# Kernel tuning notes

Measured on AMD Instinct MI355X. Metric: run time of the kernel, lower is better.

## Reference

```python
import jax, jax.numpy as jnp
import numpy as np

# TensorProductConvLayer (DiffDock-style): gather -> edge-MLP-weighted fully
# connected tensor product (lmax=1 irreps) -> scatter-mean.
# in/out irreps: ns x0e + nv x1o + nv x1e + ns x0o ; sh irreps: 1x0e + 1x1o
NS, NV = 16, 4
N_NODES, N_EDGES = 8000, 160000
EDGE_FEAT = 3 * NS                      # 48
IRREPS_DIM = 2 * NS + 6 * NV            # 56
# per-path weight block sizes (fully-connected 'uvw' paths, mul2 = 1):
# [A:0e*0e->0e, B:1o*1o->0e, A:0e*1o->1o, B:1o*0e->1o, C:1e*1o->1o,
#  B:1o*1o->1e, C:1e*0e->1e, D:0o*1o->1e, C:1e*1o->0o, D:0o*0e->0o]
PATH_SIZES = [NS*NS, NV*NS, NS*NV, NV*NV, NV*NV, NV*NV, NV*NV, NS*NV, NV*NS, NS*NS]
W_NUMEL = sum(PATH_SIZES)               # 832
# component-normalized CG factors: 1x1->0 uses delta/sqrt(3); 1x1->1 uses eps/sqrt(2)
INV_SQRT3 = float(1.0 / np.sqrt(3.0))
INV_SQRT2 = float(1.0 / np.sqrt(2.0))
# element path normalization: 1/sqrt(total fan-in mul per output irrep)
A_SCAL = float(1.0 / np.sqrt(NS + NV))      # 0e / 0o outputs
A_VEC = float(1.0 / np.sqrt(NS + 2 * NV))   # 1o / 1e outputs


def setup_inputs() -> dict:
    key = jax.random.key(0)
    ks = jax.random.split(key, 6)
    node_attr = jax.random.normal(ks[0], (N_NODES, IRREPS_DIM), jnp.float32)
    edge_index = jax.random.randint(ks[1], (2, N_EDGES), 0, N_NODES)
    edge_attr = jax.random.normal(ks[2], (N_EDGES, EDGE_FEAT), jnp.float32)
    edge_sh = jax.random.normal(ks[3], (N_EDGES, 4), jnp.float32)
    s = float(1.0 / np.sqrt(EDGE_FEAT))
    fc_w1 = jax.random.normal(ks[4], (EDGE_FEAT, EDGE_FEAT), jnp.float32) * s
    fc_b1 = jnp.zeros((EDGE_FEAT,), jnp.float32)
    fc_w2 = jax.random.normal(ks[5], (EDGE_FEAT, W_NUMEL), jnp.float32) * s
    fc_b2 = jnp.zeros((W_NUMEL,), jnp.float32)
    return dict(node_attr=node_attr, edge_attr=edge_attr, edge_sh=edge_sh,
                fc_w1=fc_w1, fc_b1=fc_b1, fc_w2=fc_w2, fc_b2=fc_b2,
                edge_index=edge_index)


def _split_weights(w):
    outs, off = [], 0
    for sz in PATH_SIZES:
        outs.append(w[:, off:off + sz])
        off += sz
    return outs


def _tp_conv(node_attr, edge_attr, edge_sh, fc_w1, fc_b1, fc_w2, fc_b2, src, dst):
    # edge MLP -> per-edge tensor-product weights [E, 832]
    h = jax.nn.relu(edge_attr @ fc_w1 + fc_b1)
    w = h @ fc_w2 + fc_b2
    wA0, wB0, wA1, wB1, wC1, wB1e, wC1e, wD1e, wC0o, wD0o = _split_weights(w)

    x = node_attr[dst]                         # gather [E, 56]
    x0e = x[:, :NS]
    x1o = x[:, NS:NS + 3 * NV].reshape(-1, NV, 3)
    x1e = x[:, NS + 3 * NV:NS + 6 * NV].reshape(-1, NV, 3)
    x0o = x[:, NS + 6 * NV:]
    s0 = edge_sh[:, 0]
    s1 = edge_sh[:, 1:4]

    # ---- 0e output [E, ns]
    o0e = jnp.einsum('eu,euv->ev', x0e, wA0.reshape(-1, NS, NS)) * s0[:, None]
    dot_b = jnp.einsum('eui,ei->eu', x1o, s1) * INV_SQRT3   # 1o x 1o -> 0e
    o0e = (o0e + jnp.einsum('eu,euv->ev', dot_b, wB0.reshape(-1, NV, NS))) * A_SCAL

    # ---- 1o output [E, nv, 3]
    o1o = jnp.einsum('eu,euv->ev', x0e, wA1.reshape(-1, NS, NV))[:, :, None] * s1[:, None, :]
    o1o = o1o + jnp.einsum('eui,euv->evi', x1o, wB1.reshape(-1, NV, NV)) * s0[:, None, None]
    cr_e = jnp.cross(x1e, s1[:, None, :]) * INV_SQRT2       # 1e x 1o -> 1o
    o1o = (o1o + jnp.einsum('eui,euv->evi', cr_e, wC1.reshape(-1, NV, NV))) * A_VEC

    # ---- 1e output [E, nv, 3]
    cr_o = jnp.cross(x1o, s1[:, None, :]) * INV_SQRT2       # 1o x 1o -> 1e
    o1e = jnp.einsum('eui,euv->evi', cr_o, wB1e.reshape(-1, NV, NV))
    o1e = o1e + jnp.einsum('eui,euv->evi', x1e, wC1e.reshape(-1, NV, NV)) * s0[:, None, None]
    o1e = (o1e + jnp.einsum('eu,euv->ev', x0o, wD1e.reshape(-1, NS, NV))[:, :, None] * s1[:, None, :]) * A_VEC

    # ---- 0o output [E, ns]
    dot_c = jnp.einsum('eui,ei->eu', x1e, s1) * INV_SQRT3   # 1e x 1o -> 0o
    o0o = jnp.einsum('eu,euv->ev', dot_c, wC0o.reshape(-1, NV, NS))
    o0o = (o0o + jnp.einsum('eu,euv->ev', x0o, wD0o.reshape(-1, NS, NS)) * s0[:, None]) * A_SCAL

    tp = jnp.concatenate([o0e, o1o.reshape(-1, 3 * NV), o1e.reshape(-1, 3 * NV), o0o], axis=-1)

    # scatter-mean over source nodes
    summed = jax.ops.segment_sum(tp, src, num_segments=N_NODES)
    counts = jax.ops.segment_sum(jnp.ones((tp.shape[0],), tp.dtype), src, num_segments=N_NODES)
    return summed / jnp.maximum(counts, 1.0)[:, None]


def reference(node_attr, edge_attr, edge_sh, fc_w1, fc_b1, fc_w2, fc_b2, edge_index):
    src, dst = edge_index[0], edge_index[1]
    return _tp_conv(node_attr, edge_attr, edge_sh, fc_w1, fc_b1, fc_w2, fc_b2, src, dst)
```

## Files before the change

kernel.cpp:

```cpp
#include <hip/hip_runtime.h>
#include <hip/hip_fp16.h>

#define IRR    56
#define EF     48
#define WN     832
#define NEDGE  160000
#define NNODE  8000
#define NT     512
#define TE2    64
#define NTASK  (NEDGE / TE2)
#define GRID   NTASK

#define INV_SQRT3 0.5773502691896258f
#define INV_SQRT2 0.7071067811865476f
#define A_SCAL    0.22360679774997896f
#define A_VEC     0.20412414523193154f

typedef __bf16 bf16x8 __attribute__((ext_vector_type(8)));
typedef float  f32x4  __attribute__((ext_vector_type(4)));
typedef unsigned short u16x8 __attribute__((ext_vector_type(8)));
typedef unsigned short u16x4 __attribute__((ext_vector_type(4)));

__device__ __forceinline__ unsigned short f2bf(float f) {
    unsigned int u = __builtin_bit_cast(unsigned int, f);
    u += 0x7FFFu + ((u >> 16) & 1u);
    return (unsigned short)(u >> 16);
}

__global__ void k_setup(const float* __restrict__ w1, const float* __restrict__ b1,
                        const float* __restrict__ w2, const float* __restrict__ b2,
                        unsigned short* __restrict__ W1T, unsigned short* __restrict__ W2L,
                        const int* __restrict__ edge_index, int* __restrict__ hist)
{
    int o = blockIdx.x * 256 + threadIdx.x;
    if (o < 64 * 832) {
        int k = o / 832;
        int n = o - k * 832;
        float v = (k < EF) ? w2[k * WN + n] : ((k == EF) ? b2[n] : 0.f);
        int i = n >> 4, mm = n & 15;
        int f = k >> 5, q = (k >> 3) & 3, j = k & 7;
        int o2 = (((i * 2 + f) * 64) + (q * 16 + mm)) * 8 + j;
        W2L[o2] = f2bf(v);
    }
    if (o < EF * EF) { int k = o / EF, n = o - k * EF; W1T[n * 64 + k] = f2bf(w1[o]); }
    if (o < EF * 16) { int n = o >> 4, kk = EF + (o & 15); W1T[n * 64 + kk] = (kk == EF) ? f2bf(b1[n]) : (unsigned short)0; }
    if (o < NEDGE) atomicAdd(&hist[edge_index[o]], 1);
}

__global__ __launch_bounds__(NT, 4) void tp_fused(
    const float* __restrict__ node_attr,
    const float* __restrict__ edge_attr,
    const float* __restrict__ edge_sh,
    const int*   __restrict__ edge_index,
    const int*   __restrict__ hist,
    const unsigned short* __restrict__ W1T,
    const unsigned short* __restrict__ W2L,
    float* __restrict__ out)
{
    __shared__ __align__(16) unsigned char UGH[TE2 * 56 * 4];
    __shared__ __align__(16) float sF0[TE2 * 61];
    __shared__ __align__(16) float sF1[TE2 * 61];
    __shared__ __align__(16) float sO[TE2 * IRR];
    __shared__ int   sSrc[TE2], sDst[TE2];
    __shared__ float sInv[TE2];

    float*          sG = (float*)UGH;
    unsigned short* sH = (unsigned short*)UGH;

    const int tid   = threadIdx.x;
    const int lane  = tid & 63;
    const int wv    = tid >> 6;
    const int half  = wv >> 2;
    const int wl    = wv & 3;
    const int m     = lane & 15;
    const int quad  = lane >> 4;
    const int em    = wl * 16 + m;
    const int e0    = blockIdx.x * TE2;

    if (tid < TE2)          sSrc[tid]       = edge_index[e0 + tid];
    else if (tid < 2 * TE2) sDst[tid - TE2] = edge_index[NEDGE + e0 + tid - TE2];
    __syncthreads();

    {
        const float* nrow = node_attr + (size_t)sDst[em] * IRR;
        float* g = sG + em * 56;
        if (half == 0) {
            *(float4*)(g + quad * 4)        = *(const float4*)(nrow + quad * 4);
            *(float4*)(g + (quad + 4) * 4)  = *(const float4*)(nrow + (quad + 4) * 4);
        } else {
            *(float4*)(g + (quad + 8) * 4)  = *(const float4*)(nrow + (quad + 8) * 4);
            if (quad < 2) { int c = 12 + quad; *(float4*)(g + c * 4) = *(const float4*)(nrow + c * 4); }
        }
    }
    if (tid >= 256 && tid < 256 + TE2) {
        int e = tid - 256;
        sInv[e] = 1.0f / fmaxf((float)hist[sSrc[e]], 1.0f);
    }

    float4 sh4 = *(const float4*)&edge_sh[(size_t)(e0 + em) * 4];
    const float s0 = sh4.x, sx = sh4.y, sy = sh4.z, sz = sh4.w;

    __syncthreads();

    {
        const float* x = sG + em * 56;
        const float c0S = s0 * A_SCAL;
        const float c0V = s0 * A_VEC;
        const float cD3 = INV_SQRT3 * A_SCAL;
        const float cC2 = INV_SQRT2 * A_VEC;
        if (half == 0) {
            float* F = sF0 + em * 61;
            #pragma unroll
            for (int t = 0; t < 4; t++) {
                int u = quad * 4 + t;
                float x0e = x[u];
                F[u]      = x0e * c0S;
                F[20 + u] = x0e * A_VEC;
            }
            {
                int u = quad;
                float a0 = x[16 + u*3], a1 = x[16 + u*3 + 1], a2 = x[16 + u*3 + 2];
                float b0 = x[28 + u*3], b1 = x[28 + u*3 + 1], b2 = x[28 + u*3 + 2];
                F[16 + u] = (a0*sx + a1*sy + a2*sz) * cD3;
                F[36 + u*3 + 0] = a0 * c0V;
                F[36 + u*3 + 1] = a1 * c0V;
                F[36 + u*3 + 2] = a2 * c0V;
                F[48 + u*3 + 0] = (b1*sz - b2*sy) * cC2;
                F[48 + u*3 + 1] = (b2*sx - b0*sz) * cC2;
                F[48 + u*3 + 2] = (b0*sy - b1*sx) * cC2;
            }
        } else {
            float* F = sF1 + em * 61;
            {
                int u = quad;
                float a0 = x[16 + u*3], a1 = x[16 + u*3 + 1], a2 = x[16 + u*3 + 2];
                float b0 = x[28 + u*3], b1 = x[28 + u*3 + 1], b2 = x[28 + u*3 + 2];
                F[u*3 + 0]      = (a1*sz - a2*sy) * cC2;
                F[u*3 + 1]      = (a2*sx - a0*sz) * cC2;
                F[u*3 + 2]      = (a0*sy - a1*sx) * cC2;
                F[12 + u*3 + 0] = b0 * c0V;
                F[12 + u*3 + 1] = b1 * c0V;
                F[12 + u*3 + 2] = b2 * c0V;
                F[40 + u]       = (b0*sx + b1*sy + b2*sz) * cD3;
            }
            #pragma unroll
            for (int t = 0; t < 4; t++) {
                int u = quad * 4 + t;
                float x0o = x[40 + u];
                F[24 + u] = x0o * A_VEC;
                F[44 + u] = x0o * c0S;
            }
        }
    }

    bf16x8 hb0, hb1;
    if (half == 0) {
        const float* arow = edge_attr + (size_t)(e0 + em) * EF;
        float av0[8], av1[8];
        {
            float4 p0 = *(const float4*)(arow + quad * 8);
            float4 p1 = *(const float4*)(arow + quad * 8 + 4);
            av0[0]=p0.x; av0[1]=p0.y; av0[2]=p0.z; av0[3]=p0.w;
            av0[4]=p1.x; av0[5]=p1.y; av0[6]=p1.z; av0[7]=p1.w;
        }
        if (quad < 2) {
            float4 p0 = *(const float4*)(arow + 32 + quad * 8);
            float4 p1 = *(const float4*)(arow + 32 + quad * 8 + 4);
            av1[0]=p0.x; av1[1]=p0.y; av1[2]=p0.z; av1[3]=p0.w;
            av1[4]=p1.x; av1[5]=p1.y; av1[6]=p1.z; av1[7]=p1.w;
        } else {
            #pragma unroll
            for (int j = 0; j < 8; j++) av1[j] = 0.f;
            if (quad == 2) av1[0] = 1.f;
        }
        u16x8 ub0, ub1;
        #pragma unroll
        for (int j = 0; j < 8; j++) { ub0[j] = f2bf(av0[j]); ub1[j] = f2bf(av1[j]); }
        hb0 = __builtin_bit_cast(bf16x8, ub0);
        hb1 = __builtin_bit_cast(bf16x8, ub1);
    }

    __syncthreads();

    if (half == 0) {
        #pragma unroll
        for (int nth = 0; nth < 3; nth++) {
            bf16x8 a0 = __builtin_bit_cast(bf16x8, *(const u16x8*)&W1T[(nth*16 + m)*64 + quad*8]);
            bf16x8 a1 = __builtin_bit_cast(bf16x8, *(const u16x8*)&W1T[(nth*16 + m)*64 + 32 + quad*8]);
            f32x4 c = {0.f, 0.f, 0.f, 0.f};
            c = __builtin_amdgcn_mfma_f32_16x16x32_bf16(a0, hb0, c, 0, 0, 0);
            c = __builtin_amdgcn_mfma_f32_16x16x32_bf16(a1, hb1, c, 0, 0, 0);
            u16x4 hp;
            #pragma unroll
            for (int r = 0; r < 4; r++) hp[r] = f2bf(fmaxf(c[r], 0.f));
            *(u16x4*)&sH[em * 72 + nth*16 + quad*4] = hp;
        }
        if (quad == 3) {
            u16x4 b = {0x3F80, 0, 0, 0}, z = {0, 0, 0, 0};
            *(u16x4*)&sH[em * 72 + 48] = b;
            *(u16x4*)&sH[em * 72 + 52] = z;
            *(u16x4*)&sH[em * 72 + 56] = z;
            *(u16x4*)&sH[em * 72 + 60] = z;
        }
    }
    __syncthreads();

    bf16x8 HB0 = __builtin_bit_cast(bf16x8, *(const u16x8*)&sH[em * 72 + quad*8]);
    bf16x8 HB1 = __builtin_bit_cast(bf16x8, *(const u16x8*)&sH[em * 72 + 32 + quad*8]);

    const unsigned short* Wt = W2L + (size_t)half * 26 * 1024;

    if (half == 0) {
        const float* Fp = sF0 + em * 61;
        float oe[4] = {0.f,0.f,0.f,0.f};
        float sA[4] = {0.f,0.f,0.f,0.f};
        float t1[12] = {0.f,0.f,0.f,0.f,0.f,0.f,0.f,0.f,0.f,0.f,0.f,0.f};
        #pragma unroll
        for (int i = 0; i < 26; i++) {
            u16x8 Af = *(const u16x8*)&Wt[i * 1024 + lane * 8];
            u16x8 Bf = *(const u16x8*)&Wt[i * 1024 + 512 + lane * 8];
            f32x4 c = {0.f,0.f,0.f,0.f};
            c = __builtin_amdgcn_mfma_f32_16x16x32_bf16(__builtin_bit_cast(bf16x8, Af), HB0, c, 0, 0, 0);
            c = __builtin_amdgcn_mfma_f32_16x16x32_bf16(__builtin_bit_cast(bf16x8, Bf), HB1, c, 0, 0, 0);
            if (i < 20) {
                float f = Fp[i];
                #pragma unroll
                for (int r = 0; r < 4; r++) oe[r] += f * c[r];
            } else if (i < 24) {
                float f = Fp[20 + (i - 20)*4 + quad];
                #pragma unroll
                for (int r = 0; r < 4; r++) sA[r] += f * c[r];
            } else {
                int u = (i - 24)*4 + quad;
                #pragma unroll
                for (int i3 = 0; i3 < 3; i3++) {
                    float f = Fp[36 + u*3 + i3];
                    #pragma unroll
                    for (int r = 0; r < 4; r++) t1[i3*4 + r] += f * c[r];
                }
            }
        }
        #pragma unroll
        for (int r = 0; r < 4; r++) {
            sA[r] += __shfl_xor(sA[r], 16, 64);  sA[r] += __shfl_xor(sA[r], 32, 64);
        }
        #pragma unroll
        for (int i = 0; i < 12; i++) {
            t1[i] += __shfl_xor(t1[i], 16, 64);  t1[i] += __shfl_xor(t1[i], 32, 64);
        }
        float4 v0; v0.x = oe[0]; v0.y = oe[1]; v0.z = oe[2]; v0.w = oe[3];
        *(float4*)&sO[em * IRR + quad*4] = v0;
        if (quad == 0) {
            #pragma unroll
            for (int r = 0; r < 4; r++) {
                sO[em * IRR + 16 + r*3 + 0] = sA[r] * sx + t1[0*4 + r];
                sO[em * IRR + 16 + r*3 + 1] = sA[r] * sy + t1[1*4 + r];
                sO[em * IRR + 16 + r*3 + 2] = sA[r] * sz + t1[2*4 + r];
            }
        }
    } else {
        const float* Fp = sF1 + em * 61;
        float sD[4] = {0.f,0.f,0.f,0.f};
        float t1[12] = {0.f,0.f,0.f,0.f,0.f,0.f,0.f,0.f,0.f,0.f,0.f,0.f};
        float oo[4] = {0.f,0.f,0.f,0.f};
        #pragma unroll
        for (int i = 0; i < 26; i++) {
            u16x8 Af = *(const u16x8*)&Wt[i * 1024 + lane * 8];
            u16x8 Bf = *(const u16x8*)&Wt[i * 1024 + 512 + lane * 8];
            f32x4 c = {0.f,0.f,0.f,0.f};
            c = __builtin_amdgcn_mfma_f32_16x16x32_bf16(__builtin_bit_cast(bf16x8, Af), HB0, c, 0, 0, 0);
            c = __builtin_amdgcn_mfma_f32_16x16x32_bf16(__builtin_bit_cast(bf16x8, Bf), HB1, c, 0, 0, 0);
            if (i < 2) {
                int j = i*4 + quad;
                #pragma unroll
                for (int i3 = 0; i3 < 3; i3++) {
                    float f = Fp[j*3 + i3];
                    #pragma unroll
                    for (int r = 0; r < 4; r++) t1[i3*4 + r] += f * c[r];
                }
            } else if (i < 6) {
                float f = Fp[24 + (i - 2)*4 + quad];
                #pragma unroll
                for (int r = 0; r < 4; r++) sD[r] += f * c[r];
            } else {
                float f = Fp[40 + (i - 6)];
                #pragma unroll
                for (int r = 0; r < 4; r++) oo[r] += f * c[r];
            }
        }
        #pragma unroll
        for (int r = 0; r < 4; r++) {
            sD[r] += __shfl_xor(sD[r], 16, 64);  sD[r] += __shfl_xor(sD[r], 32, 64);
        }
        #pragma unroll
        for (int i = 0; i < 12; i++) {
            t1[i] += __shfl_xor(t1[i], 16, 64);  t1[i] += __shfl_xor(t1[i], 32, 64);
        }
        float4 v1; v1.x = oo[0]; v1.y = oo[1]; v1.z = oo[2]; v1.w = oo[3];
        *(float4*)&sO[em * IRR + 28 + 12 + quad*4] = v1;
        if (quad == 0) {
            #pragma unroll
            for (int r = 0; r < 4; r++) {
                sO[em * IRR + 28 + r*3 + 0] = sD[r] * sx + t1[0*4 + r];
                sO[em * IRR + 28 + r*3 + 1] = sD[r] * sy + t1[1*4 + r];
                sO[em * IRR + 28 + r*3 + 2] = sD[r] * sz + t1[2*4 + r];
            }
        }
    }

    __syncthreads();

    #pragma unroll
    for (int it = 0; it < 7; it++) {
        int idx = it * NT + tid;
        int e = idx / IRR, ch = idx - e * IRR;
        unsafeAtomicAdd(&out[(size_t)sSrc[e] * IRR + ch], sO[e * IRR + ch] * sInv[e]);
    }
}

extern "C" void kernel_launch(void* const* d_in, const int* in_sizes, int n_in,
                              void* d_out, int out_size, void* d_ws, size_t ws_size,
                              hipStream_t stream) {
    const float* node_attr  = (const float*)d_in[0];
    const float* edge_attr  = (const float*)d_in[1];
    const float* edge_sh    = (const float*)d_in[2];
    const float* fc_w1      = (const float*)d_in[3];
    const float* fc_b1      = (const float*)d_in[4];
    const float* fc_w2      = (const float*)d_in[5];
    const float* fc_b2      = (const float*)d_in[6];
    const int*   edge_index = (const int*)d_in[7];

    int* hist = (int*)d_ws;
    unsigned short* W1T = (unsigned short*)(hist + NNODE);
    unsigned short* W2L = W1T + EF * 64;

    hipMemsetAsync(hist, 0, NNODE * sizeof(int), stream);
    hipMemsetAsync(d_out, 0, (size_t)out_size * sizeof(float), stream);

    k_setup<<<(NEDGE + 255) / 256, 256, 0, stream>>>(
        fc_w1, fc_b1, fc_w2, fc_b2, W1T, W2L, edge_index, hist);

    tp_fused<<<GRID, NT, 0, stream>>>(node_attr, edge_attr, edge_sh, edge_index,
                                      hist, W1T, W2L, (float*)d_out);
}
```

Before: 168.7 us.

## Prefetch W2 fragments into registers and atomically scatter directly from registers

```diff
diff --git a/kernel.cpp b/kernel.cpp
--- a/kernel.cpp
+++ b/kernel.cpp
@@ -57,15 +57,12 @@
     const unsigned short* __restrict__ W2L,
     float* __restrict__ out)
 {
-    __shared__ __align__(16) unsigned char UGH[TE2 * 56 * 4];
+    __shared__ __align__(16) float sG[TE2 * 56];
+    __shared__ __align__(16) unsigned short sH[TE2 * 72];
     __shared__ __align__(16) float sF0[TE2 * 61];
     __shared__ __align__(16) float sF1[TE2 * 61];
-    __shared__ __align__(16) float sO[TE2 * IRR];
     __shared__ int   sSrc[TE2], sDst[TE2];
     __shared__ float sInv[TE2];
-
-    float*          sG = (float*)UGH;
-    unsigned short* sH = (unsigned short*)UGH;
 
     const int tid   = threadIdx.x;
     const int lane  = tid & 63;
@@ -153,6 +150,8 @@
         }
     }
 
+    const unsigned short* Wt = W2L + (size_t)half * 26 * 1024;
+
     bf16x8 hb0, hb1;
     if (half == 0) {
         const float* arow = edge_attr + (size_t)(e0 + em) * EF;
@@ -178,11 +177,7 @@
         for (int j = 0; j < 8; j++) { ub0[j] = f2bf(av0[j]); ub1[j] = f2bf(av1[j]); }
         hb0 = __builtin_bit_cast(bf16x8, ub0);
         hb1 = __builtin_bit_cast(bf16x8, ub1);
-    }
-
-    __syncthreads();
-
-    if (half == 0) {
+
         #pragma unroll
         for (int nth = 0; nth < 3; nth++) {
             bf16x8 a0 = __builtin_bit_cast(bf16x8, *(const u16x8*)&W1T[(nth*16 + m)*64 + quad*8]);
@@ -203,12 +198,20 @@
             *(u16x4*)&sH[em * 72 + 60] = z;
         }
     }
+
+    u16x8 AFr[8], BFr[8];
+    #pragma unroll
+    for (int p = 0; p < 8; p++) {
+        AFr[p] = *(const u16x8*)&Wt[p * 1024 + lane * 8];
+        BFr[p] = *(const u16x8*)&Wt[p * 1024 + 512 + lane * 8];
+    }
+
     __syncthreads();
 
     bf16x8 HB0 = __builtin_bit_cast(bf16x8, *(const u16x8*)&sH[em * 72 + quad*8]);
     bf16x8 HB1 = __builtin_bit_cast(bf16x8, *(const u16x8*)&sH[em * 72 + 32 + quad*8]);
-
-    const unsigned short* Wt = W2L + (size_t)half * 26 * 1024;
+    const float inv = sInv[em];
+    float* orow = out + (size_t)sSrc[em] * IRR;
 
     if (half == 0) {
         const float* Fp = sF0 + em * 61;
@@ -217,8 +220,12 @@
         float t1[12] = {0.f,0.f,0.f,0.f,0.f,0.f,0.f,0.f,0.f,0.f,0.f,0.f};
         #pragma unroll
         for (int i = 0; i < 26; i++) {
-            u16x8 Af = *(const u16x8*)&Wt[i * 1024 + lane * 8];
-            u16x8 Bf = *(const u16x8*)&Wt[i * 1024 + 512 + lane * 8];
+            u16x8 Af = AFr[i & 7];
+            u16x8 Bf = BFr[i & 7];
+            if (i + 8 < 26) {
+                AFr[i & 7] = *(const u16x8*)&Wt[(i + 8) * 1024 + lane * 8];
+                BFr[i & 7] = *(const u16x8*)&Wt[(i + 8) * 1024 + 512 + lane * 8];
+            }
             f32x4 c = {0.f,0.f,0.f,0.f};
             c = __builtin_amdgcn_mfma_f32_16x16x32_bf16(__builtin_bit_cast(bf16x8, Af), HB0, c, 0, 0, 0);
             c = __builtin_amdgcn_mfma_f32_16x16x32_bf16(__builtin_bit_cast(bf16x8, Bf), HB1, c, 0, 0, 0);
@@ -248,15 +255,14 @@
         for (int i = 0; i < 12; i++) {
             t1[i] += __shfl_xor(t1[i], 16, 64);  t1[i] += __shfl_xor(t1[i], 32, 64);
         }
-        float4 v0; v0.x = oe[0]; v0.y = oe[1]; v0.z = oe[2]; v0.w = oe[3];
-        *(float4*)&sO[em * IRR + quad*4] = v0;
-        if (quad == 0) {
-            #pragma unroll
-            for (int r = 0; r < 4; r++) {
-                sO[em * IRR + 16 + r*3 + 0] = sA[r] * sx + t1[0*4 + r];
-                sO[em * IRR + 16 + r*3 + 1] = sA[r] * sy + t1[1*4 + r];
-                sO[em * IRR + 16 + r*3 + 2] = sA[r] * sz + t1[2*4 + r];
-            }
+        #pragma unroll
+        for (int r = 0; r < 4; r++)
+            unsafeAtomicAdd(&orow[quad*4 + r], oe[r] * inv);
+        #pragma unroll
+        for (int q = 0; q < 4; q++) if (quad == q) {
+            unsafeAtomicAdd(&orow[16 + q*3 + 0], (sA[q]*sx + t1[0*4 + q]) * inv);
+            unsafeAtomicAdd(&orow[16 + q*3 + 1], (sA[q]*sy + t1[1*4 + q]) * inv);
+            unsafeAtomicAdd(&orow[16 + q*3 + 2], (sA[q]*sz + t1[2*4 + q]) * inv);
         }
     } else {
         const float* Fp = sF1 + em * 61;
@@ -265,8 +271,12 @@
         float oo[4] = {0.f,0.f,0.f,0.f};
         #pragma unroll
         for (int i = 0; i < 26; i++) {
-            u16x8 Af = *(const u16x8*)&Wt[i * 1024 + lane * 8];
-            u16x8 Bf = *(const u16x8*)&Wt[i * 1024 + 512 + lane * 8];
+            u16x8 Af = AFr[i & 7];
+            u16x8 Bf = BFr[i & 7];
+            if (i + 8 < 26) {
+                AFr[i & 7] = *(const u16x8*)&Wt[(i + 8) * 1024 + lane * 8];
+                BFr[i & 7] = *(const u16x8*)&Wt[(i + 8) * 1024 + 512 + lane * 8];
+            }
             f32x4 c = {0.f,0.f,0.f,0.f};
             c = __builtin_amdgcn_mfma_f32_16x16x32_bf16(__builtin_bit_cast(bf16x8, Af), HB0, c, 0, 0, 0);
             c = __builtin_amdgcn_mfma_f32_16x16x32_bf16(__builtin_bit_cast(bf16x8, Bf), HB1, c, 0, 0, 0);
@@ -296,25 +306,15 @@
         for (int i = 0; i < 12; i++) {
             t1[i] += __shfl_xor(t1[i], 16, 64);  t1[i] += __shfl_xor(t1[i], 32, 64);
         }
-        float4 v1; v1.x = oo[0]; v1.y = oo[1]; v1.z = oo[2]; v1.w = oo[3];
-        *(float4*)&sO[em * IRR + 28 + 12 + quad*4] = v1;
-        if (quad == 0) {
-            #pragma unroll
-            for (int r = 0; r < 4; r++) {
-                sO[em * IRR + 28 + r*3 + 0] = sD[r] * sx + t1[0*4 + r];
-                sO[em * IRR + 28 + r*3 + 1] = sD[r] * sy + t1[1*4 + r];
-                sO[em * IRR + 28 + r*3 + 2] = sD[r] * sz + t1[2*4 + r];
-            }
-        }
-    }
-
-    __syncthreads();
-
-    #pragma unroll
-    for (int it = 0; it < 7; it++) {
-        int idx = it * NT + tid;
-        int e = idx / IRR, ch = idx - e * IRR;
-        unsafeAtomicAdd(&out[(size_t)sSrc[e] * IRR + ch], sO[e * IRR + ch] * sInv[e]);
+        #pragma unroll
+        for (int r = 0; r < 4; r++)
+            unsafeAtomicAdd(&orow[40 + quad*4 + r], oo[r] * inv);
+        #pragma unroll
+        for (int q = 0; q < 4; q++) if (quad == q) {
+            unsafeAtomicAdd(&orow[28 + q*3 + 0], (sD[q]*sx + t1[0*4 + q]) * inv);
+            unsafeAtomicAdd(&orow[28 + q*3 + 1], (sD[q]*sy + t1[1*4 + q]) * inv);
+            unsafeAtomicAdd(&orow[28 + q*3 + 2], (sD[q]*sz + t1[2*4 + q]) * inv);
+        }
     }
 }
 
```

After: 332.6 us. 97.1% more time.

## Split W2 tile work across waves with register-resident weights, loop over edge groups

Applied to the files above, without the earlier changes.

```diff
diff --git a/kernel.cpp b/kernel.cpp
--- a/kernel.cpp
+++ b/kernel.cpp
@@ -47,7 +47,27 @@
     if (o < NEDGE) atomicAdd(&hist[edge_index[o]], 1);
 }
 
-__global__ __launch_bounds__(NT, 4) void tp_fused(
+#define MM2(C, WA, WB) do { \
+    C = __builtin_amdgcn_mfma_f32_16x16x32_bf16(__builtin_bit_cast(bf16x8, WA), HB0g, C, 0, 0, 0); \
+    C = __builtin_amdgcn_mfma_f32_16x16x32_bf16(__builtin_bit_cast(bf16x8, WB), HB1g, C, 0, 0, 0); \
+} while (0)
+
+#define OE_T(WA, WB, FV) do { f32x4 c = {0.f,0.f,0.f,0.f}; MM2(c, WA, WB); float f = (FV); \
+    o0 += f*c[0]; o1 += f*c[1]; o2 += f*c[2]; o3 += f*c[3]; } while (0)
+
+#define SA_T(WA, WB, FIDX) do { f32x4 c = {0.f,0.f,0.f,0.f}; MM2(c, WA, WB); float f = Fg[FIDX]; \
+    sA[0] += f*c[0]; sA[1] += f*c[1]; sA[2] += f*c[2]; sA[3] += f*c[3]; } while (0)
+
+#define T1_T(WA, WB, U, BASE) do { f32x4 c = {0.f,0.f,0.f,0.f}; MM2(c, WA, WB); \
+    _Pragma("unroll") for (int i3 = 0; i3 < 3; i3++) { float f = Fg[(BASE) + (U)*3 + i3]; \
+    _Pragma("unroll") for (int r = 0; r < 4; r++) t1[i3*4 + r] += f*c[r]; } } while (0)
+
+#define RED16() do { \
+    _Pragma("unroll") for (int r = 0; r < 4; r++) { sA[r] += __shfl_xor(sA[r], 16, 64); sA[r] += __shfl_xor(sA[r], 32, 64); } \
+    _Pragma("unroll") for (int i = 0; i < 12; i++) { t1[i] += __shfl_xor(t1[i], 16, 64); t1[i] += __shfl_xor(t1[i], 32, 64); } \
+} while (0)
+
+__global__ __launch_bounds__(NT, 2) void tp_fused(
     const float* __restrict__ node_attr,
     const float* __restrict__ edge_attr,
     const float* __restrict__ edge_sh,
@@ -57,15 +77,14 @@
     const unsigned short* __restrict__ W2L,
     float* __restrict__ out)
 {
-    __shared__ __align__(16) unsigned char UGH[TE2 * 56 * 4];
+    __shared__ __align__(16) float sG[TE2 * 56];
+    __shared__ __align__(16) unsigned short sH[TE2 * 72];
     __shared__ __align__(16) float sF0[TE2 * 61];
     __shared__ __align__(16) float sF1[TE2 * 61];
     __shared__ __align__(16) float sO[TE2 * IRR];
+    __shared__ __align__(16) float4 sS1v[TE2];
     __shared__ int   sSrc[TE2], sDst[TE2];
     __shared__ float sInv[TE2];
-
-    float*          sG = (float*)UGH;
-    unsigned short* sH = (unsigned short*)UGH;
 
     const int tid   = threadIdx.x;
     const int lane  = tid & 63;
@@ -77,6 +96,23 @@
     const int em    = wl * 16 + m;
     const int e0    = blockIdx.x * TE2;
 
+    const unsigned short* Wt = W2L + (size_t)half * 26 * 1024;
+    int tb, tn7, special;
+    if (half == 0) { tb = (wl == 0) ? 0 : (wl == 1) ? 7 : (wl == 2) ? 14 : 20; tn7 = (wl < 2); special = (wl == 3); }
+    else           { tb = (wl == 0) ? 0 : (wl == 1) ? 6 : (wl == 2) ? 13 : 20; tn7 = (wl == 1 || wl == 2); special = (wl == 0); }
+    const unsigned short* Wp = Wt + tb * 1024 + lane * 8;
+    const int o6 = (tn7 ? 6 : 5) * 1024;
+    u16x8 w0A = *(const u16x8*)&Wp[0];        u16x8 w0B = *(const u16x8*)&Wp[512];
+    u16x8 w1A = *(const u16x8*)&Wp[1024];     u16x8 w1B = *(const u16x8*)&Wp[1024 + 512];
+    u16x8 w2A = *(const u16x8*)&Wp[2048];     u16x8 w2B = *(const u16x8*)&Wp[2048 + 512];
+    u16x8 w3A = *(const u16x8*)&Wp[3072];     u16x8 w3B = *(const u16x8*)&Wp[3072 + 512];
+    u16x8 w4A = *(const u16x8*)&Wp[4096];     u16x8 w4B = *(const u16x8*)&Wp[4096 + 512];
+    u16x8 w5A = *(const u16x8*)&Wp[5120];     u16x8 w5B = *(const u16x8*)&Wp[5120 + 512];
+    u16x8 w6A = *(const u16x8*)&Wp[o6];       u16x8 w6B = *(const u16x8*)&Wp[o6 + 512];
+
+    #pragma unroll
+    for (int it = 0; it < 7; it++) sO[it * NT + tid] = 0.f;
+
     if (tid < TE2)          sSrc[tid]       = edge_index[e0 + tid];
     else if (tid < 2 * TE2) sDst[tid - TE2] = edge_index[NEDGE + e0 + tid - TE2];
     __syncthreads();
@@ -99,6 +135,7 @@
 
     float4 sh4 = *(const float4*)&edge_sh[(size_t)(e0 + em) * 4];
     const float s0 = sh4.x, sx = sh4.y, sy = sh4.z, sz = sh4.w;
+    if (half == 0 && quad == 0) sS1v[em] = sh4;
 
     __syncthreads();
 
@@ -153,7 +190,6 @@
         }
     }
 
-    bf16x8 hb0, hb1;
     if (half == 0) {
         const float* arow = edge_attr + (size_t)(e0 + em) * EF;
         float av0[8], av1[8];
@@ -176,13 +212,9 @@
         u16x8 ub0, ub1;
         #pragma unroll
         for (int j = 0; j < 8; j++) { ub0[j] = f2bf(av0[j]); ub1[j] = f2bf(av1[j]); }
-        hb0 = __builtin_bit_cast(bf16x8, ub0);
-        hb1 = __builtin_bit_cast(bf16x8, ub1);
-    }
-
-    __syncthreads();
-
-    if (half == 0) {
+        bf16x8 hb0 = __builtin_bit_cast(bf16x8, ub0);
+        bf16x8 hb1 = __builtin_bit_cast(bf16x8, ub1);
+
         #pragma unroll
         for (int nth = 0; nth < 3; nth++) {
             bf16x8 a0 = __builtin_bit_cast(bf16x8, *(const u16x8*)&W1T[(nth*16 + m)*64 + quad*8]);
@@ -205,105 +237,79 @@
     }
     __syncthreads();
 
-    bf16x8 HB0 = __builtin_bit_cast(bf16x8, *(const u16x8*)&sH[em * 72 + quad*8]);
-    bf16x8 HB1 = __builtin_bit_cast(bf16x8, *(const u16x8*)&sH[em * 72 + 32 + quad*8]);
-
-    const unsigned short* Wt = W2L + (size_t)half * 26 * 1024;
-
-    if (half == 0) {
-        const float* Fp = sF0 + em * 61;
-        float oe[4] = {0.f,0.f,0.f,0.f};
-        float sA[4] = {0.f,0.f,0.f,0.f};
-        float t1[12] = {0.f,0.f,0.f,0.f,0.f,0.f,0.f,0.f,0.f,0.f,0.f,0.f};
-        #pragma unroll
-        for (int i = 0; i < 26; i++) {
-            u16x8 Af = *(const u16x8*)&Wt[i * 1024 + lane * 8];
-            u16x8 Bf = *(const u16x8*)&Wt[i * 1024 + 512 + lane * 8];
-            f32x4 c = {0.f,0.f,0.f,0.f};
-            c = __builtin_amdgcn_mfma_f32_16x16x32_bf16(__builtin_bit_cast(bf16x8, Af), HB0, c, 0, 0, 0);
-            c = __builtin_amdgcn_mfma_f32_16x16x32_bf16(__builtin_bit_cast(bf16x8, Bf), HB1, c, 0, 0, 0);
-            if (i < 20) {
-                float f = Fp[i];
+    const float* sFme = (half == 0) ? sF0 : sF1;
+    const int fb  = (half == 0) ? tb : tb + 34;
+    const int chb = (half == 0) ? 0 : 40;
+
+    if (!special) {
+        #pragma unroll
+        for (int g = 0; g < 4; g++) {
+            const int eg = g * 16 + m;
+            bf16x8 HB0g = __builtin_bit_cast(bf16x8, *(const u16x8*)&sH[eg * 72 + quad*8]);
+            bf16x8 HB1g = __builtin_bit_cast(bf16x8, *(const u16x8*)&sH[eg * 72 + 32 + quad*8]);
+            const float* Fg = sFme + eg * 61;
+            float o0 = 0.f, o1 = 0.f, o2 = 0.f, o3 = 0.f;
+            OE_T(w0A, w0B, Fg[fb + 0]);
+            OE_T(w1A, w1B, Fg[fb + 1]);
+            OE_T(w2A, w2B, Fg[fb + 2]);
+            OE_T(w3A, w3B, Fg[fb + 3]);
+            OE_T(w4A, w4B, Fg[fb + 4]);
+            OE_T(w5A, w5B, Fg[fb + 5]);
+            OE_T(w6A, w6B, tn7 ? Fg[fb + 6] : 0.f);
+            float* p = sO + eg * IRR + chb + quad * 4;
+            atomicAdd(p + 0, o0); atomicAdd(p + 1, o1);
+            atomicAdd(p + 2, o2); atomicAdd(p + 3, o3);
+        }
+    } else if (half == 0) {
+        #pragma unroll
+        for (int g = 0; g < 4; g++) {
+            const int eg = g * 16 + m;
+            bf16x8 HB0g = __builtin_bit_cast(bf16x8, *(const u16x8*)&sH[eg * 72 + quad*8]);
+            bf16x8 HB1g = __builtin_bit_cast(bf16x8, *(const u16x8*)&sH[eg * 72 + 32 + quad*8]);
+            const float* Fg = sFme + eg * 61;
+            float sA[4] = {0.f,0.f,0.f,0.f};
+            float t1[12] = {0.f,0.f,0.f,0.f,0.f,0.f,0.f,0.f,0.f,0.f,0.f,0.f};
+            SA_T(w0A, w0B, 20 + 0*4 + quad);
+            SA_T(w1A, w1B, 20 + 1*4 + quad);
+            SA_T(w2A, w2B, 20 + 2*4 + quad);
+            SA_T(w3A, w3B, 20 + 3*4 + quad);
+            T1_T(w4A, w4B, quad, 36);
+            T1_T(w5A, w5B, 4 + quad, 36);
+            RED16();
+            float4 s1g = sS1v[eg];
+            if (quad == 0) {
                 #pragma unroll
-                for (int r = 0; r < 4; r++) oe[r] += f * c[r];
-            } else if (i < 24) {
-                float f = Fp[20 + (i - 20)*4 + quad];
+                for (int r = 0; r < 4; r++) {
+                    sO[eg * IRR + 16 + r*3 + 0] = sA[r] * s1g.y + t1[0*4 + r];
+                    sO[eg * IRR + 16 + r*3 + 1] = sA[r] * s1g.z + t1[1*4 + r];
+                    sO[eg * IRR + 16 + r*3 + 2] = sA[r] * s1g.w + t1[2*4 + r];
+                }
+            }
+        }
+    } else {
+        #pragma unroll
+        for (int g = 0; g < 4; g++) {
+            const int eg = g * 16 + m;
+            bf16x8 HB0g = __builtin_bit_cast(bf16x8, *(const u16x8*)&sH[eg * 72 + quad*8]);
+            bf16x8 HB1g = __builtin_bit_cast(bf16x8, *(const u16x8*)&sH[eg * 72 + 32 + quad*8]);
+            const float* Fg = sFme + eg * 61;
+            float sA[4] = {0.f,0.f,0.f,0.f};
+            float t1[12] = {0.f,0.f,0.f,0.f,0.f,0.f,0.f,0.f,0.f,0.f,0.f,0.f};
+            T1_T(w0A, w0B, quad, 0);
+            T1_T(w1A, w1B, 4 + quad, 0);
+            SA_T(w2A, w2B, 24 + 0*4 + quad);
+            SA_T(w3A, w3B, 24 + 1*4 + quad);
+            SA_T(w4A, w4B, 24 + 2*4 + quad);
+            SA_T(w5A, w5B, 24 + 3*4 + quad);
+            RED16();
+            float4 s1g = sS1v[eg];
+            if (quad == 0) {
                 #pragma unroll
-                for (int r = 0; r < 4; r++) sA[r] += f * c[r];
-            } else {
-                int u = (i - 24)*4 + quad;
-                #pragma unroll
-                for (int i3 = 0; i3 < 3; i3++) {
-                    float f = Fp[36 + u*3 + i3];
-                    #pragma unroll
-                    for (int r = 0; r < 4; r++) t1[i3*4 + r] += f * c[r];
+                for (int r = 0; r < 4; r++) {
+                    sO[eg * IRR + 28 + r*3 + 0] = sA[r] * s1g.y + t1[0*4 + r];
+                    sO[eg * IRR + 28 + r*3 + 1] = sA[r] * s1g.z + t1[1*4 + r];
+                    sO[eg * IRR + 28 + r*3 + 2] = sA[r] * s1g.w + t1[2*4 + r];
                 }
-            }
-        }
-        #pragma unroll
-        for (int r = 0; r < 4; r++) {
-            sA[r] += __shfl_xor(sA[r], 16, 64);  sA[r] += __shfl_xor(sA[r], 32, 64);
-        }
-        #pragma unroll
-        for (int i = 0; i < 12; i++) {
-            t1[i] += __shfl_xor(t1[i], 16, 64);  t1[i] += __shfl_xor(t1[i], 32, 64);
-        }
-        float4 v0; v0.x = oe[0]; v0.y = oe[1]; v0.z = oe[2]; v0.w = oe[3];
-        *(float4*)&sO[em * IRR + quad*4] = v0;
-        if (quad == 0) {
-            #pragma unroll
-            for (int r = 0; r < 4; r++) {
-                sO[em * IRR + 16 + r*3 + 0] = sA[r] * sx + t1[0*4 + r];
-                sO[em * IRR + 16 + r*3 + 1] = sA[r] * sy + t1[1*4 + r];
-                sO[em * IRR + 16 + r*3 + 2] = sA[r] * sz + t1[2*4 + r];
-            }
-        }
-    } else {
-        const float* Fp = sF1 + em * 61;
-        float sD[4] = {0.f,0.f,0.f,0.f};
-        float t1[12] = {0.f,0.f,0.f,0.f,0.f,0.f,0.f,0.f,0.f,0.f,0.f,0.f};
-        float oo[4] = {0.f,0.f,0.f,0.f};
-        #pragma unroll
-        for (int i = 0; i < 26; i++) {
-            u16x8 Af = *(const u16x8*)&Wt[i * 1024 + lane * 8];
-            u16x8 Bf = *(const u16x8*)&Wt[i * 1024 + 512 + lane * 8];
-            f32x4 c = {0.f,0.f,0.f,0.f};
-            c = __builtin_amdgcn_mfma_f32_16x16x32_bf16(__builtin_bit_cast(bf16x8, Af), HB0, c, 0, 0, 0);
-            c = __builtin_amdgcn_mfma_f32_16x16x32_bf16(__builtin_bit_cast(bf16x8, Bf), HB1, c, 0, 0, 0);
-            if (i < 2) {
-                int j = i*4 + quad;
-                #pragma unroll
-                for (int i3 = 0; i3 < 3; i3++) {
-                    float f = Fp[j*3 + i3];
-                    #pragma unroll
-                    for (int r = 0; r < 4; r++) t1[i3*4 + r] += f * c[r];
-                }
-            } else if (i < 6) {
-                float f = Fp[24 + (i - 2)*4 + quad];
-                #pragma unroll
-                for (int r = 0; r < 4; r++) sD[r] += f * c[r];
-            } else {
-                float f = Fp[40 + (i - 6)];
-                #pragma unroll
-                for (int r = 0; r < 4; r++) oo[r] += f * c[r];
-            }
-        }
-        #pragma unroll
-        for (int r = 0; r < 4; r++) {
-            sD[r] += __shfl_xor(sD[r], 16, 64);  sD[r] += __shfl_xor(sD[r], 32, 64);
-        }
-        #pragma unroll
-        for (int i = 0; i < 12; i++) {
-            t1[i] += __shfl_xor(t1[i], 16, 64);  t1[i] += __shfl_xor(t1[i], 32, 64);
-        }
-        float4 v1; v1.x = oo[0]; v1.y = oo[1]; v1.z = oo[2]; v1.w = oo[3];
-        *(float4*)&sO[em * IRR + 28 + 12 + quad*4] = v1;
-        if (quad == 0) {
-            #pragma unroll
-            for (int r = 0; r < 4; r++) {
-                sO[em * IRR + 28 + r*3 + 0] = sD[r] * sx + t1[0*4 + r];
-                sO[em * IRR + 28 + r*3 + 1] = sD[r] * sy + t1[1*4 + r];
-                sO[em * IRR + 28 + r*3 + 2] = sD[r] * sz + t1[2*4 + r];
             }
         }
     }
```

New measurement: 233.8 us. 38.6% more time.
